# Performance work log

Hardware: AMD Instinct MI355X
Metric: run time of the kernel (lower is better)

The kernel has to match this reference:

```python
import jax, jax.numpy as jnp
import numpy as np

B, S, D = 2, 4096, 512
H = 8
W = 512            # local attention window size
HD = D // H        # head dim
NC = S // W        # number of chunks
HALF = W // 2      # symmetric half-window


def setup_inputs() -> dict:
    key = jax.random.key(0)
    ks = jax.random.split(key, 12)
    s = 1.0 / np.sqrt(D)
    return {
        "val": jax.random.normal(ks[0], (B, S, D), jnp.float32),
        "Wq": jax.random.normal(ks[1], (D, D), jnp.float32) * s,
        "bq": jnp.zeros((D,), jnp.float32),
        "Wk": jax.random.normal(ks[2], (D, D), jnp.float32) * s,
        "bk": jnp.zeros((D,), jnp.float32),
        "Wv": jax.random.normal(ks[3], (D, D), jnp.float32) * s,
        "bv": jnp.zeros((D,), jnp.float32),
        "Wo": jax.random.normal(ks[4], (D, D), jnp.float32) * s,
        "bo": jnp.zeros((D,), jnp.float32),
        "gamma": jnp.ones((D,), jnp.float32),
        "beta": jnp.zeros((D,), jnp.float32),
    }


def _heads(x):
    # [B,S,D] -> [B,H,S,HD]
    return x.reshape(B, S, H, HD).transpose(0, 2, 1, 3)


def _gather_neighbors(x):
    # x: [B,H,S,HD] -> [B,H,NC,3W,HD] (prev | cur | next chunk, zero-padded at ends)
    xp = jnp.pad(x, ((0, 0), (0, 0), (W, W), (0, 0)))
    xc = xp.reshape(B, H, NC + 2, W, HD)
    return jnp.concatenate([xc[:, :, :-2], xc[:, :, 1:-1], xc[:, :, 2:]], axis=3)


def _local_attention(x, Wq, bq, Wk, bk, Wv, bv, Wo, bo):
    q = _heads(x @ Wq + bq)
    k = _heads(x @ Wk + bk)
    v = _heads(x @ Wv + bv)

    qc = q.reshape(B, H, NC, W, HD)            # chunked queries
    kn = _gather_neighbors(k)                  # [B,H,NC,3W,HD]
    vn = _gather_neighbors(v)

    scale = 1.0 / np.sqrt(HD)
    scores = jnp.einsum("bhcqd,bhckd->bhcqk", qc, kn) * scale  # [B,H,NC,W,3W]

    # banded mask: key relative position in [-HALF, HALF], and key index in [0,S)
    qi = jnp.arange(W)[:, None]
    kj = jnp.arange(3 * W)[None, :]
    band = jnp.abs(kj - W - qi) <= HALF                          # [W,3W]
    key_pos = (jnp.arange(NC)[:, None, None] - 1) * W + kj[None]  # [NC,1,3W]
    valid = (key_pos >= 0) & (key_pos < S)                       # [NC,1,3W]
    mask = band[None] & valid                                    # [NC,W,3W]

    scores = jnp.where(mask[None, None], scores, jnp.float32(-1e9))
    p = jax.nn.softmax(scores, axis=-1)
    o = jnp.einsum("bhcqk,bhckd->bhcqd", p, vn)                  # [B,H,NC,W,HD]
    o = o.reshape(B, H, S, HD).transpose(0, 2, 1, 3).reshape(B, S, D)
    return o @ Wo + bo


def _layer_norm(x, gamma, beta, eps=1e-5):
    mu = jnp.mean(x, axis=-1, keepdims=True)
    var = jnp.mean(jnp.square(x - mu), axis=-1, keepdims=True)
    return (x - mu) * jax.lax.rsqrt(var + eps) * gamma + beta


def reference(val, Wq, bq, Wk, bk, Wv, bv, Wo, bo, gamma, beta):
    attn_out = _local_attention(val, Wq, bq, Wk, bk, Wv, bv, Wo, bo)
    return _layer_norm(val + attn_out, gamma, beta)
```

## Files before the change

kernel.cpp:

```cpp
#include <hip/hip_runtime.h>
#include <hip/hip_bf16.h>

#define BATCH 2
#define SEQ   4096
#define DIM   512
#define NHEAD 8
#define HDIM  64
#define ROWS  (BATCH*SEQ)

typedef float  fx4   __attribute__((ext_vector_type(4)));
typedef __bf16 bf16x8 __attribute__((ext_vector_type(8)));
typedef unsigned short ushort_t;
typedef unsigned short usx4 __attribute__((ext_vector_type(4)));
typedef unsigned short usx8 __attribute__((ext_vector_type(8)));

static __device__ __forceinline__ float b2f(ushort_t v) {
    union { unsigned int u; float f; } c; c.u = ((unsigned int)v) << 16; return c.f;
}
static __device__ __forceinline__ ushort_t f2b(float f) {
    union { float f; unsigned int u; } c; c.f = f;
    unsigned int u = c.u;
    unsigned int r = (u + 0x7FFFu + ((u >> 16) & 1u)) >> 16;
    return (ushort_t)r;
}
static __device__ __forceinline__ void gload16(const ushort_t* g, ushort_t* l) {
    __builtin_amdgcn_global_load_lds(
        (const __attribute__((address_space(1))) unsigned int*)g,
        (__attribute__((address_space(3))) unsigned int*)l, 16, 0, 0);
}

__global__ __launch_bounds__(256) void prep_kernel(
    const float* __restrict__ val, ushort_t* __restrict__ xb,
    const float* __restrict__ W0, const float* __restrict__ W1,
    const float* __restrict__ W2, const float* __restrict__ W3,
    ushort_t* __restrict__ T0, ushort_t* __restrict__ T1,
    ushort_t* __restrict__ T2, ushort_t* __restrict__ T3) {

    const int tid = threadIdx.x;
    if (blockIdx.y == 4) {
        const int stride = 64 * 256 * 4;
        for (int i = (blockIdx.x * 256 + tid) * 4; i < ROWS * 512; i += stride) {
            fx4 v = *(const fx4*)(val + i);
            usx4 o; o.x = f2b(v.x); o.y = f2b(v.y); o.z = f2b(v.z); o.w = f2b(v.w);
            *(usx4*)(xb + i) = o;
        }
        return;
    }
    const float* W; ushort_t* WT;
    switch (blockIdx.y) {
        case 0: W = W0; WT = T0; break;
        case 1: W = W1; WT = T1; break;
        case 2: W = W2; WT = T2; break;
        default: W = W3; WT = T3; break;
    }
    __shared__ float tile[64][65];
    int r0 = (blockIdx.x & 7) * 64;
    int c0 = (blockIdx.x >> 3) * 64;
    for (int idx = tid; idx < 4096; idx += 256) {
        int rr = idx >> 6, cc = idx & 63;
        tile[rr][cc] = W[(c0 + rr) * 512 + (r0 + cc)];
    }
    __syncthreads();
    for (int idx = tid; idx < 4096; idx += 256) {
        int rr = idx >> 6, cc = idx & 63;
        WT[(size_t)(r0 + rr) * 512 + (c0 + cc)] = f2b(tile[cc][rr]);
    }
}

__global__ __launch_bounds__(256) void gemm128_kernel(
    const ushort_t* __restrict__ A,
    const ushort_t* __restrict__ BT0, const ushort_t* __restrict__ BT1, const ushort_t* __restrict__ BT2,
    const float* __restrict__ b0, const float* __restrict__ b1, const float* __restrict__ b2,
    ushort_t* __restrict__ C0, ushort_t* __restrict__ C1, ushort_t* __restrict__ C2) {

    const ushort_t* BT; const float* bias; ushort_t* C;
    if (blockIdx.z == 0)      { BT = BT0; bias = b0; C = C0; }
    else if (blockIdx.z == 1) { BT = BT1; bias = b1; C = C1; }
    else                      { BT = BT2; bias = b2; C = C2; }

    __shared__ ushort_t As[2][128 * 32];
    __shared__ ushort_t Bs[2][128 * 32];

    const int tid  = threadIdx.x;
    const int wave = tid >> 6;
    const int lane = tid & 63;
    const int lm   = lane & 15;
    const int quad = lane >> 4;
    const int wm   = wave >> 1;
    const int wn   = wave & 1;

    const int m0t = blockIdx.x * 128;
    const int n0t = blockIdx.y * 128;

    const int srow = tid >> 2, sgc = tid & 3;
    const ushort_t* ga0 = A  + (size_t)(m0t + srow) * 512 + sgc * 8;
    const ushort_t* ga1 = ga0 + (size_t)64 * 512;
    const ushort_t* gb0 = BT + (size_t)(n0t + srow) * 512 + sgc * 8;
    const ushort_t* gb1 = gb0 + (size_t)64 * 512;

    const int aoff = (wm * 64 + lm) * 32 + quad * 8;
    const int boff = (wn * 64 + lm) * 32 + quad * 8;

    fx4 acc[4][4];
    #pragma unroll
    for (int i = 0; i < 4; ++i)
        #pragma unroll
        for (int j = 0; j < 4; ++j) acc[i][j] = 0;

    gload16(ga0, &As[0][tid * 8]);
    gload16(ga1, &As[0][(tid + 256) * 8]);
    gload16(gb0, &Bs[0][tid * 8]);
    gload16(gb1, &Bs[0][(tid + 256) * 8]);

    for (int it = 0; it < 16; ++it) {
        const int cur = it & 1, nxt = cur ^ 1;
        __syncthreads();
        if (it < 15) {
            const int k0 = (it + 1) * 32;
            gload16(ga0 + k0, &As[nxt][tid * 8]);
            gload16(ga1 + k0, &As[nxt][(tid + 256) * 8]);
            gload16(gb0 + k0, &Bs[nxt][tid * 8]);
            gload16(gb1 + k0, &Bs[nxt][(tid + 256) * 8]);
        }
        bf16x8 af[4], bfr[4];
        #pragma unroll
        for (int ms = 0; ms < 4; ++ms) af[ms]  = *(const bf16x8*)&As[cur][aoff + ms * 512];
        #pragma unroll
        for (int ns = 0; ns < 4; ++ns) bfr[ns] = *(const bf16x8*)&Bs[cur][boff + ns * 512];
        #pragma unroll
        for (int ms = 0; ms < 4; ++ms)
            #pragma unroll
            for (int ns = 0; ns < 4; ++ns)
                acc[ms][ns] = __builtin_amdgcn_mfma_f32_16x16x32_bf16(af[ms], bfr[ns], acc[ms][ns], 0, 0, 0);
    }

    const int crow0 = m0t + wm * 64 + quad * 4;
    const int ccol0 = n0t + wn * 64 + lm;

    if (blockIdx.z == 2) {
        #pragma unroll
        for (int ns = 0; ns < 4; ++ns) {
            int col = ccol0 + ns * 16;
            int h = col >> 6, d = col & 63;
            float bv = bias[col];
            #pragma unroll
            for (int ms = 0; ms < 4; ++ms) {
                int m = crow0 + ms * 16;
                int bb = m >> 12, s0 = m & 4095;
                usx4 o;
                o.x = f2b(acc[ms][ns][0] + bv); o.y = f2b(acc[ms][ns][1] + bv);
                o.z = f2b(acc[ms][ns][2] + bv); o.w = f2b(acc[ms][ns][3] + bv);
                *(usx4*)(C + (((size_t)(bb * 8 + h) * 64 + d) * 4096 + s0)) = o;
            }
        }
    } else {
        #pragma unroll
        for (int ns = 0; ns < 4; ++ns) {
            int col = ccol0 + ns * 16;
            float bv = bias[col];
            #pragma unroll
            for (int ms = 0; ms < 4; ++ms) {
                #pragma unroll
                for (int r = 0; r < 4; ++r) {
                    C[(size_t)(crow0 + ms * 16 + r) * 512 + col] = f2b(acc[ms][ns][r] + bv);
                }
            }
        }
    }
}

__global__ __launch_bounds__(256) void attn_mfma_kernel(
    const ushort_t* __restrict__ Qb, const ushort_t* __restrict__ Kb,
    const ushort_t* __restrict__ Vt, ushort_t* __restrict__ Ob) {

    __shared__ ushort_t Klds[64 * 64];
    __shared__ ushort_t Vlds[64 * 64];
    __shared__ ushort_t Plds[4 * 32 * 72];

    const int tid  = threadIdx.x;
    const int wave = tid >> 6;
    const int lane = tid & 63;
    const int lm   = lane & 15;
    const int quad = lane >> 4;

    const int bh = blockIdx.y;
    const int b = bh >> 3, h = bh & 7;
    const int q0 = blockIdx.x * 128;
    const int qw = q0 + wave * 32;

    bf16x8 qf[2][2];
    #pragma unroll
    for (int qs = 0; qs < 2; ++qs) {
        const ushort_t* qp = Qb + ((size_t)(b * SEQ + qw + qs * 16 + lm)) * 512 + h * 64 + quad * 8;
        qf[qs][0] = *(const bf16x8*)qp;
        qf[qs][1] = *(const bf16x8*)(qp + 32);
    }

    int koff[2][4], voff[2][4];
    #pragma unroll
    for (int ks = 0; ks < 2; ++ks) {
        #pragma unroll
        for (int tn = 0; tn < 4; ++tn) {
            int key = tn * 16 + lm;
            koff[ks][tn] = key * 64 + (((ks * 4 + quad) ^ (key & 7)) * 8);
            int d = tn * 16 + lm;
            voff[ks][tn] = d * 64 + (((ks * 4 + quad) ^ (d & 7)) * 8);
        }
    }
    ushort_t* Pw = Plds + wave * (32 * 72);
    int pread[2][2];
    #pragma unroll
    for (int qs = 0; qs < 2; ++qs)
        #pragma unroll
        for (int ks = 0; ks < 2; ++ks)
            pread[qs][ks] = (qs * 16 + lm) * 72 + ks * 32 + quad * 8;

    const int skey = tid >> 3;
    const int sdg  = tid & 7;
    const size_t kgbase = ((size_t)b * SEQ) * 512 + h * 64 + sdg * 8;
    const size_t vgbase = ((size_t)bh * 64) * 4096 + sdg * 8;
    const int l0 = skey * 64 + ((sdg ^ (skey & 7)) * 8);
    const int l1 = l0 + 32 * 64;

    const int klo = (q0 >= 256) ? 0 : ((256 - q0) >> 6);
    const int khi = min(9, (4288 - q0) >> 6);
    const int wlo = wave >> 1, whi = 8 + (wave >> 1);
    const int flo = 1 + (wave >> 1), fhi = 7 + (wave >> 1);

    bf16x8 onesf;
    {
        __bf16 o = (lm == 0) ? (__bf16)1.0f : (__bf16)0.0f;
        #pragma unroll
        for (int j = 0; j < 8; ++j) onesf[j] = o;
    }

    fx4 oacc[2][4];
    #pragma unroll
    for (int qs = 0; qs < 2; ++qs)
        #pragma unroll
        for (int tn = 0; tn < 4; ++tn) oacc[qs][tn] = 0;
    fx4 lacc[2];
    lacc[0] = 0; lacc[1] = 0;

    usx8 kn0, kn1, vn0, vn1;
    {
        int ts = q0 - 256 + klo * 64;
        kn0 = *(const usx8*)(Kb + kgbase + (size_t)(ts + skey) * 512);
        kn1 = *(const usx8*)(Kb + kgbase + (size_t)(ts + skey + 32) * 512);
        vn0 = *(const usx8*)(Vt + vgbase + (size_t)skey * 4096 + ts);
        vn1 = *(const usx8*)(Vt + vgbase + (size_t)(skey + 32) * 4096 + ts);
    }

    for (int kt = klo; kt <= khi; ++kt) {
        const int ts = q0 - 256 + kt * 64;
        __syncthreads();
        *(usx8*)&Klds[l0] = kn0;
        *(usx8*)&Klds[l1] = kn1;
        *(usx8*)&Vlds[l0] = vn0;
        *(usx8*)&Vlds[l1] = vn1;
        __syncthreads();

        if (kt < khi) {
            int t2 = ts + 64;
            kn0 = *(const usx8*)(Kb + kgbase + (size_t)(t2 + skey) * 512);
            kn1 = *(const usx8*)(Kb + kgbase + (size_t)(t2 + skey + 32) * 512);
            vn0 = *(const usx8*)(Vt + vgbase + (size_t)skey * 4096 + t2);
            vn1 = *(const usx8*)(Vt + vgbase + (size_t)(skey + 32) * 4096 + t2);
        }

        if (kt < wlo || kt > whi) continue;

        bf16x8 kf[2][4];
        #pragma unroll
        for (int ks = 0; ks < 2; ++ks)
            #pragma unroll
            for (int tn = 0; tn < 4; ++tn)
                kf[ks][tn] = *(const bf16x8*)&Klds[koff[ks][tn]];
        fx4 sacc[2][4];
        #pragma unroll
        for (int qs = 0; qs < 2; ++qs)
            #pragma unroll
            for (int tn = 0; tn < 4; ++tn) sacc[qs][tn] = 0;
        #pragma unroll
        for (int ks = 0; ks < 2; ++ks)
            #pragma unroll
            for (int tn = 0; tn < 4; ++tn) {
                sacc[0][tn] = __builtin_amdgcn_mfma_f32_16x16x32_bf16(qf[0][ks], kf[ks][tn], sacc[0][tn], 0, 0, 0);
                sacc[1][tn] = __builtin_amdgcn_mfma_f32_16x16x32_bf16(qf[1][ks], kf[ks][tn], sacc[1][tn], 0, 0, 0);
            }

        const bool edge = (kt < flo) || (kt > fhi);
        #pragma unroll
        for (int qs = 0; qs < 2; ++qs) {
            #pragma unroll
            for (int tn = 0; tn < 4; ++tn) {
                int kg = ts + tn * 16 + lm;
                #pragma unroll
                for (int r = 0; r < 4; ++r) {
                    float p = __expf(sacc[qs][tn][r] * 0.125f);
                    if (edge) {
                        int dlt = kg - (qw + qs * 16 + quad * 4 + r);
                        p = (dlt <= 256 && dlt >= -256) ? p : 0.0f;
                    }
                    Pw[(qs * 16 + quad * 4 + r) * 72 + tn * 16 + lm] = f2b(p);
                }
            }
        }

        bf16x8 vf[2][4];
        #pragma unroll
        for (int ks = 0; ks < 2; ++ks)
            #pragma unroll
            for (int tn = 0; tn < 4; ++tn)
                vf[ks][tn] = *(const bf16x8*)&Vlds[voff[ks][tn]];
        #pragma unroll
        for (int qs = 0; qs < 2; ++qs) {
            #pragma unroll
            for (int ks = 0; ks < 2; ++ks) {
                bf16x8 ap = *(const bf16x8*)&Pw[pread[qs][ks]];
                lacc[qs] = __builtin_amdgcn_mfma_f32_16x16x32_bf16(ap, onesf, lacc[qs], 0, 0, 0);
                #pragma unroll
                for (int tn = 0; tn < 4; ++tn)
                    oacc[qs][tn] = __builtin_amdgcn_mfma_f32_16x16x32_bf16(ap, vf[ks][tn], oacc[qs][tn], 0, 0, 0);
            }
        }
    }

    #pragma unroll
    for (int qs = 0; qs < 2; ++qs) {
        float linv[4];
        #pragma unroll
        for (int r = 0; r < 4; ++r) {
            float lv = __shfl(lacc[qs][r], (lane & 48));
            linv[r] = 1.0f / lv;
        }
        ushort_t* ob = Ob + ((size_t)(b * SEQ + qw + qs * 16 + quad * 4)) * 512 + h * 64 + lm;
        #pragma unroll
        for (int tn = 0; tn < 4; ++tn)
            #pragma unroll
            for (int r = 0; r < 4; ++r)
                ob[(size_t)r * 512 + tn * 16] = f2b(oacc[qs][tn][r] * linv[r]);
    }
}

__global__ __launch_bounds__(256) void ln_kernel(
    const ushort_t* __restrict__ xb, const ushort_t* __restrict__ ob,
    const float* __restrict__ gamma, const float* __restrict__ beta,
    float* __restrict__ out) {

    int row  = blockIdx.x * 4 + (threadIdx.x >> 6);
    int lane = threadIdx.x & 63;

    const ushort_t* xp = xb + (size_t)row * 512 + lane * 8;
    const ushort_t* op = ob + (size_t)row * 512 + lane * 8;

    usx4 xa = ((const usx4*)xp)[0];
    usx4 xc = ((const usx4*)xp)[1];
    usx4 oa = ((const usx4*)op)[0];
    usx4 oc = ((const usx4*)op)[1];
    fx4 va, vb;
    va.x = b2f(xa.x) + b2f(oa.x); va.y = b2f(xa.y) + b2f(oa.y);
    va.z = b2f(xa.z) + b2f(oa.z); va.w = b2f(xa.w) + b2f(oa.w);
    vb.x = b2f(xc.x) + b2f(oc.x); vb.y = b2f(xc.y) + b2f(oc.y);
    vb.z = b2f(xc.z) + b2f(oc.z); vb.w = b2f(xc.w) + b2f(oc.w);

    float s = va.x + va.y + va.z + va.w + vb.x + vb.y + vb.z + vb.w;
    #pragma unroll
    for (int m = 32; m > 0; m >>= 1) s += __shfl_xor(s, m);
    float mu = s * (1.0f / 512.0f);

    fx4 da = va - mu;
    fx4 db = vb - mu;
    float ss = da.x*da.x + da.y*da.y + da.z*da.z + da.w*da.w
             + db.x*db.x + db.y*db.y + db.z*db.z + db.w*db.w;
    #pragma unroll
    for (int m = 32; m > 0; m >>= 1) ss += __shfl_xor(ss, m);
    float rstd = rsqrtf(ss * (1.0f / 512.0f) + 1e-5f);

    const fx4* gp = (const fx4*)(gamma + lane * 8);
    const fx4* bp = (const fx4*)(beta  + lane * 8);
    fx4 g0 = gp[0], g1 = gp[1], b0 = bp[0], b1 = bp[1];

    float* outp = out + (size_t)row * 512 + lane * 8;
    fx4 r0 = da * rstd * g0 + b0;
    fx4 r1 = db * rstd * g1 + b1;
    ((fx4*)outp)[0] = r0;
    ((fx4*)outp)[1] = r1;
}

extern "C" void kernel_launch(void* const* d_in, const int* in_sizes, int n_in,
                              void* d_out, int out_size, void* d_ws, size_t ws_size,
                              hipStream_t stream) {
    const float* val   = (const float*)d_in[0];
    const float* Wq    = (const float*)d_in[1];
    const float* bq    = (const float*)d_in[2];
    const float* Wk    = (const float*)d_in[3];
    const float* bk    = (const float*)d_in[4];
    const float* Wv    = (const float*)d_in[5];
    const float* bv    = (const float*)d_in[6];
    const float* Wo    = (const float*)d_in[7];
    const float* bo    = (const float*)d_in[8];
    const float* gamma = (const float*)d_in[9];
    const float* beta  = (const float*)d_in[10];
    float* out = (float*)d_out;

    char* w = (char*)d_ws;
    ushort_t* xb    = (ushort_t*)w; w += (size_t)ROWS * 512 * 2;
    ushort_t* WqT   = (ushort_t*)w; w += 512 * 512 * 2;
    ushort_t* WkT   = (ushort_t*)w; w += 512 * 512 * 2;
    ushort_t* WvT   = (ushort_t*)w; w += 512 * 512 * 2;
    ushort_t* WoT   = (ushort_t*)w; w += 512 * 512 * 2;
    ushort_t* Qb    = (ushort_t*)w; w += (size_t)ROWS * 512 * 2;
    ushort_t* Kb    = (ushort_t*)w; w += (size_t)ROWS * 512 * 2;
    ushort_t* Vtb   = (ushort_t*)w; w += (size_t)ROWS * 512 * 2;
    ushort_t* attnb = (ushort_t*)w; w += (size_t)ROWS * 512 * 2;
    ushort_t* obuf  = (ushort_t*)w; w += (size_t)ROWS * 512 * 2;

    prep_kernel<<<dim3(64, 5), 256, 0, stream>>>(
        val, xb, Wq, Wk, Wv, Wo, WqT, WkT, WvT, WoT);

    gemm128_kernel<<<dim3(ROWS / 128, 4, 3), 256, 0, stream>>>(
        xb, WqT, WkT, WvT, bq, bk, bv, Qb, Kb, Vtb);

    attn_mfma_kernel<<<dim3(SEQ / 128, BATCH * NHEAD), 256, 0, stream>>>(Qb, Kb, Vtb, attnb);

    gemm128_kernel<<<dim3(ROWS / 128, 4, 1), 256, 0, stream>>>(
        attnb, WoT, WoT, WoT, bo, bo, bo, obuf, obuf, obuf);

    ln_kernel<<<ROWS / 4, 256, 0, stream>>>(xb, obuf, gamma, beta, out);
}
```

Baseline: 182.5 us.

## Fuse output projection with residual add and LayerNorm; single-buffer QKV GEMM

Replaces the separate Wo GEMM and LayerNorm kernels with one kernel. Each block computes 32 full rows of the output projection, adds bias and the fp32 residual, and performs the row LayerNorm in-register with a cross-wave reduction. This removes the bf16 intermediate buffer round trip and one launch, and the residual now uses fp32 val instead of bf16 xb. The QKV GEMM is also changed from double-buffered LDS prefetch to single-buffered with two barriers per k-step, which may expose load latency. The fused kernel reloads the full 512x32 Wo slice per k-step for only 32 rows, so it does more L2 traffic per block.

```diff
diff --git a/kernel.cpp b/kernel.cpp
--- a/kernel.cpp
+++ b/kernel.cpp
@@ -78,8 +78,8 @@
     else if (blockIdx.z == 1) { BT = BT1; bias = b1; C = C1; }
     else                      { BT = BT2; bias = b2; C = C2; }
 
-    __shared__ ushort_t As[2][128 * 32];
-    __shared__ ushort_t Bs[2][128 * 32];
+    __shared__ ushort_t As[128 * 32];
+    __shared__ ushort_t Bs[128 * 32];
 
     const int tid  = threadIdx.x;
     const int wave = tid >> 6;
@@ -97,6 +97,10 @@
     const ushort_t* ga1 = ga0 + (size_t)64 * 512;
     const ushort_t* gb0 = BT + (size_t)(n0t + srow) * 512 + sgc * 8;
     const ushort_t* gb1 = gb0 + (size_t)64 * 512;
+    ushort_t* la0 = As + tid * 8;
+    ushort_t* la1 = As + (tid + 256) * 8;
+    ushort_t* lb0 = Bs + tid * 8;
+    ushort_t* lb1 = Bs + (tid + 256) * 8;
 
     const int aoff = (wm * 64 + lm) * 32 + quad * 8;
     const int boff = (wn * 64 + lm) * 32 + quad * 8;
@@ -107,26 +111,19 @@
         #pragma unroll
         for (int j = 0; j < 4; ++j) acc[i][j] = 0;
 
-    gload16(ga0, &As[0][tid * 8]);
-    gload16(ga1, &As[0][(tid + 256) * 8]);
-    gload16(gb0, &Bs[0][tid * 8]);
-    gload16(gb1, &Bs[0][(tid + 256) * 8]);
-
-    for (int it = 0; it < 16; ++it) {
-        const int cur = it & 1, nxt = cur ^ 1;
-        __syncthreads();
-        if (it < 15) {
-            const int k0 = (it + 1) * 32;
-            gload16(ga0 + k0, &As[nxt][tid * 8]);
-            gload16(ga1 + k0, &As[nxt][(tid + 256) * 8]);
-            gload16(gb0 + k0, &Bs[nxt][tid * 8]);
-            gload16(gb1 + k0, &Bs[nxt][(tid + 256) * 8]);
-        }
+    for (int k0 = 0; k0 < 512; k0 += 32) {
+        __syncthreads();
+        gload16(ga0 + k0, la0);
+        gload16(ga1 + k0, la1);
+        gload16(gb0 + k0, lb0);
+        gload16(gb1 + k0, lb1);
+        __syncthreads();
+
         bf16x8 af[4], bfr[4];
         #pragma unroll
-        for (int ms = 0; ms < 4; ++ms) af[ms]  = *(const bf16x8*)&As[cur][aoff + ms * 512];
-        #pragma unroll
-        for (int ns = 0; ns < 4; ++ns) bfr[ns] = *(const bf16x8*)&Bs[cur][boff + ns * 512];
+        for (int ms = 0; ms < 4; ++ms) af[ms]  = *(const bf16x8*)&As[aoff + ms * 512];
+        #pragma unroll
+        for (int ns = 0; ns < 4; ++ns) bfr[ns] = *(const bf16x8*)&Bs[boff + ns * 512];
         #pragma unroll
         for (int ms = 0; ms < 4; ++ms)
             #pragma unroll
@@ -343,49 +340,114 @@
     }
 }
 
-__global__ __launch_bounds__(256) void ln_kernel(
-    const ushort_t* __restrict__ xb, const ushort_t* __restrict__ ob,
+__global__ __launch_bounds__(256) void oproj_ln_kernel(
+    const ushort_t* __restrict__ A,
+    const ushort_t* __restrict__ WoT,
+    const float* __restrict__ bo,
+    const float* __restrict__ val,
     const float* __restrict__ gamma, const float* __restrict__ beta,
     float* __restrict__ out) {
 
-    int row  = blockIdx.x * 4 + (threadIdx.x >> 6);
-    int lane = threadIdx.x & 63;
-
-    const ushort_t* xp = xb + (size_t)row * 512 + lane * 8;
-    const ushort_t* op = ob + (size_t)row * 512 + lane * 8;
-
-    usx4 xa = ((const usx4*)xp)[0];
-    usx4 xc = ((const usx4*)xp)[1];
-    usx4 oa = ((const usx4*)op)[0];
-    usx4 oc = ((const usx4*)op)[1];
-    fx4 va, vb;
-    va.x = b2f(xa.x) + b2f(oa.x); va.y = b2f(xa.y) + b2f(oa.y);
-    va.z = b2f(xa.z) + b2f(oa.z); va.w = b2f(xa.w) + b2f(oa.w);
-    vb.x = b2f(xc.x) + b2f(oc.x); vb.y = b2f(xc.y) + b2f(oc.y);
-    vb.z = b2f(xc.z) + b2f(oc.z); vb.w = b2f(xc.w) + b2f(oc.w);
-
-    float s = va.x + va.y + va.z + va.w + vb.x + vb.y + vb.z + vb.w;
-    #pragma unroll
-    for (int m = 32; m > 0; m >>= 1) s += __shfl_xor(s, m);
-    float mu = s * (1.0f / 512.0f);
-
-    fx4 da = va - mu;
-    fx4 db = vb - mu;
-    float ss = da.x*da.x + da.y*da.y + da.z*da.z + da.w*da.w
-             + db.x*db.x + db.y*db.y + db.z*db.z + db.w*db.w;
-    #pragma unroll
-    for (int m = 32; m > 0; m >>= 1) ss += __shfl_xor(ss, m);
-    float rstd = rsqrtf(ss * (1.0f / 512.0f) + 1e-5f);
-
-    const fx4* gp = (const fx4*)(gamma + lane * 8);
-    const fx4* bp = (const fx4*)(beta  + lane * 8);
-    fx4 g0 = gp[0], g1 = gp[1], b0 = bp[0], b1 = bp[1];
-
-    float* outp = out + (size_t)row * 512 + lane * 8;
-    fx4 r0 = da * rstd * g0 + b0;
-    fx4 r1 = db * rstd * g1 + b1;
-    ((fx4*)outp)[0] = r0;
-    ((fx4*)outp)[1] = r1;
+    __shared__ ushort_t As[32 * 32];
+    __shared__ ushort_t Bs[512 * 32];
+    __shared__ float red1[32][4];
+    __shared__ float red2[32][4];
+
+    const int tid  = threadIdx.x;
+    const int wave = tid >> 6;
+    const int lane = tid & 63;
+    const int lm   = lane & 15;
+    const int quad = lane >> 4;
+
+    const int m0 = blockIdx.x * 32;
+
+    const ushort_t* gA = A + (size_t)(m0 + (tid >> 2)) * 512 + (tid & 3) * 8;
+    const int aoff = lm * 32 + quad * 8;
+    const int boff = (wave * 128 + lm) * 32 + quad * 8;
+
+    fx4 acc[2][8];
+    #pragma unroll
+    for (int ms = 0; ms < 2; ++ms)
+        #pragma unroll
+        for (int tn = 0; tn < 8; ++tn) acc[ms][tn] = 0;
+
+    for (int k0 = 0; k0 < 512; k0 += 32) {
+        __syncthreads();
+        if (tid < 128) gload16(gA + k0, &As[tid * 8]);
+        #pragma unroll
+        for (int p = 0; p < 8; ++p) {
+            int gidx = tid + 256 * p;
+            gload16(WoT + (size_t)(gidx >> 2) * 512 + (gidx & 3) * 8 + k0, &Bs[gidx * 8]);
+        }
+        __syncthreads();
+
+        bf16x8 af[2], bfr[8];
+        #pragma unroll
+        for (int ms = 0; ms < 2; ++ms) af[ms] = *(const bf16x8*)&As[aoff + ms * 512];
+        #pragma unroll
+        for (int tn = 0; tn < 8; ++tn) bfr[tn] = *(const bf16x8*)&Bs[boff + tn * 512];
+        #pragma unroll
+        for (int ms = 0; ms < 2; ++ms)
+            #pragma unroll
+            for (int tn = 0; tn < 8; ++tn)
+                acc[ms][tn] = __builtin_amdgcn_mfma_f32_16x16x32_bf16(af[ms], bfr[tn], acc[ms][tn], 0, 0, 0);
+    }
+
+    #pragma unroll
+    for (int ms = 0; ms < 2; ++ms) {
+        const int row = m0 + ms * 16 + quad * 4;
+        #pragma unroll
+        for (int tn = 0; tn < 8; ++tn) {
+            const int col = wave * 128 + tn * 16 + lm;
+            const float bv = bo[col];
+            #pragma unroll
+            for (int r = 0; r < 4; ++r)
+                acc[ms][tn][r] += bv + val[(size_t)(row + r) * 512 + col];
+        }
+    }
+
+    #pragma unroll
+    for (int ms = 0; ms < 2; ++ms) {
+        #pragma unroll
+        for (int r = 0; r < 4; ++r) {
+            float s1 = 0.f, s2 = 0.f;
+            #pragma unroll
+            for (int tn = 0; tn < 8; ++tn) {
+                float v = acc[ms][tn][r];
+                s1 += v; s2 += v * v;
+            }
+            #pragma unroll
+            for (int m = 8; m > 0; m >>= 1) {
+                s1 += __shfl_xor(s1, m);
+                s2 += __shfl_xor(s2, m);
+            }
+            if (lm == 0) {
+                int rl = ms * 16 + quad * 4 + r;
+                red1[rl][wave] = s1;
+                red2[rl][wave] = s2;
+            }
+        }
+    }
+    __syncthreads();
+
+    #pragma unroll
+    for (int ms = 0; ms < 2; ++ms) {
+        #pragma unroll
+        for (int r = 0; r < 4; ++r) {
+            const int rl = ms * 16 + quad * 4 + r;
+            float s1 = red1[rl][0] + red1[rl][1] + red1[rl][2] + red1[rl][3];
+            float s2 = red2[rl][0] + red2[rl][1] + red2[rl][2] + red2[rl][3];
+            float mu = s1 * (1.0f / 512.0f);
+            float var = s2 * (1.0f / 512.0f) - mu * mu;
+            float rstd = rsqrtf(var + 1e-5f);
+            float* op = out + (size_t)(m0 + rl) * 512;
+            #pragma unroll
+            for (int tn = 0; tn < 8; ++tn) {
+                int col = wave * 128 + tn * 16 + lm;
+                op[col] = (acc[ms][tn][r] - mu) * rstd * gamma[col] + beta[col];
+            }
+        }
+    }
 }
 
 extern "C" void kernel_launch(void* const* d_in, const int* in_sizes, int n_in,
@@ -414,7 +476,6 @@
     ushort_t* Kb    = (ushort_t*)w; w += (size_t)ROWS * 512 * 2;
     ushort_t* Vtb   = (ushort_t*)w; w += (size_t)ROWS * 512 * 2;
     ushort_t* attnb = (ushort_t*)w; w += (size_t)ROWS * 512 * 2;
-    ushort_t* obuf  = (ushort_t*)w; w += (size_t)ROWS * 512 * 2;
 
     prep_kernel<<<dim3(64, 5), 256, 0, stream>>>(
         val, xb, Wq, Wk, Wv, Wo, WqT, WkT, WvT, WoT);
@@ -424,8 +485,6 @@
 
     attn_mfma_kernel<<<dim3(SEQ / 128, BATCH * NHEAD), 256, 0, stream>>>(Qb, Kb, Vtb, attnb);
 
-    gemm128_kernel<<<dim3(ROWS / 128, 4, 1), 256, 0, stream>>>(
-        attnb, WoT, WoT, WoT, bo, bo, bo, obuf, obuf, obuf);
-
-    ln_kernel<<<ROWS / 4, 256, 0, stream>>>(xb, obuf, gamma, beta, out);
-}
+    oproj_ln_kernel<<<ROWS / 32, 256, 0, stream>>>(
+        attnb, WoT, bo, val, gamma, beta, out);
+}
```

Result: no change. 182.0 us (-0.3%).
